# Kernel tuning notes

Measured on AMD Instinct MI355X. Metric: run time of the kernel, lower is better.

The kernel has to match this reference:

```python
import jax, jax.numpy as jnp
import numpy as np

K = 5            # kernel_size
MAX_ORIENT = 8
MAX_LEVEL = 4
D = (K - 1) // 2  # pad amount = 2


def setup_inputs() -> dict:
    key = jax.random.key(0)
    k1, k2, k3 = jax.random.split(key, 3)
    x = jax.random.normal(k1, (32, 1, 512, 512), dtype=jnp.float32)
    fwd_f = jax.random.normal(k2, (MAX_ORIENT, 1, K, K), dtype=jnp.float32)
    fwd_f = fwd_f.at[0, 0].set(jnp.ones((K, K), dtype=jnp.float32))  # per __init__
    inv_f = jax.random.normal(k3, (MAX_ORIENT, 1, K, K), dtype=jnp.float32)
    return {"x": x, "forward_filters": fwd_f, "inverse_filters": inv_f}


def _pad_for_tconv(p):
    # faithful port of padding_for_transpose_conv (static python ints)
    ip, op = 0, 0
    if p > 0:
        op = p
    elif p < 0:
        a = -p
        if a % 2 == 0:
            ip = a // 2
        else:
            op = 1
            ip = (a + 1) // 2
    return ip, op


def _conv2d(x, w, stride, pad):
    # torch F.pad(x, (d,d,d,d)) then conv2d(stride) == conv with symmetric padding
    return jax.lax.conv_general_dilated(
        x, w, window_strides=(stride, stride),
        padding=((pad, pad), (pad, pad)),
        dimension_numbers=("NCHW", "OIHW", "NCHW"))


def _conv_transpose2d(x, w, stride, pad, out_pad):
    # torch conv_transpose2d, weight layout (in_ch, out_ch, kH, kW).
    # Equivalent direct conv: flip kernel spatially, swap I/O axes,
    # lhs_dilation=stride, padding lo=k-1-p, hi=k-1-p+output_padding.
    k = w.shape[2]
    w2 = jnp.transpose(jnp.flip(w, (2, 3)), (1, 0, 2, 3))  # OIHW (1,8,5,5)
    padding = tuple((k - 1 - p, k - 1 - p + op) for p, op in zip(pad, out_pad))
    return jax.lax.conv_general_dilated(
        x, w2, window_strides=(1, 1), padding=padding,
        lhs_dilation=(stride, stride),
        dimension_numbers=("NCHW", "OIHW", "NCHW"))


def _forward_transform(x, fwd_f):
    result = [None] * (MAX_LEVEL + 1)
    vimg = x
    level = MAX_LEVEL
    res = None
    while level > 0 and vimg.shape[2] > 1 and vimg.shape[3] > 1:
        res = _conv2d(vimg, fwd_f, 2, D)   # (B, 8, ceil(H/2)+?, ...)
        result[level] = res
        vimg = res[:, :1]                  # lowpass band feeds next level
        level -= 1
    result[0] = res[:, :1]
    return result


def _inverse_transform(coeffs, inp_dim, inv_f):
    rec = coeffs[0]
    for level in range(1, MAX_LEVEL + 1):
        cur = np.array(coeffs[level].shape[2:])
        target = np.array(inp_dim) if level == MAX_LEVEL else np.array(coeffs[level + 1].shape[2:])
        pc = target - 2 * (cur - 1) - K
        ip0, op0 = _pad_for_tconv(int(pc[0]))
        ip1, op1 = _pad_for_tconv(int(pc[1]))
        full = jnp.concatenate([rec, coeffs[level][:, 1:]], axis=1)  # (B,8,h,w)
        rec = _conv_transpose2d(full, inv_f, 2, (ip0, ip1), (op0, op1))
    return rec


def reference(x, forward_filters, inverse_filters):
    coeffs = _forward_transform(x, forward_filters)
    return _inverse_transform(coeffs, x.shape[2:], inverse_filters)
```

## Files before the change

kernel.cpp:

```cpp
#include <hip/hip_runtime.h>

#define NORIENT 8

__device__ __forceinline__ unsigned xcd_swz(unsigned bid, unsigned nwg) {
    unsigned chunk = nwg >> 3;
    return (nwg & 7u) ? bid : (bid & 7u) * chunk + (bid >> 3);
}

__global__ void fwd_conv_wave_kernel(const float* __restrict__ in, long in_img_stride,
                                     const float* __restrict__ filt,
                                     float* __restrict__ out,
                                     int H, int W, int OH, int OW, int N) {
    constexpr int SROW = 104;
    __shared__ float tile[67 * SROW];

    int nbx = OW >> 5, nby = OH >> 5;
    unsigned sb = xcd_swz(blockIdx.x, gridDim.x);
    int bx = (int)(sb % nbx);
    unsigned t = sb / nbx;
    int by = (int)(t % nby);
    int n = (int)(t / nby);

    const float* __restrict__ ip = in + (long)n * in_img_stride;
    int tid = threadIdx.x;

    int w = __builtin_amdgcn_readfirstlane(tid >> 6);
    const float* __restrict__ F = filt + w * 25;
    float Wt[25];
#pragma unroll
    for (int k = 0; k < 25; ++k) Wt[k] = F[k];

    int gy0 = 64 * by - 2, gx0 = 64 * bx - 4;
#pragma unroll
    for (int k = 0; k < 3; ++k) {
        int e = tid + k * 512;
        if (e < 67 * 18) {
            int row = e / 18, m = e - row * 18;
            int gy = gy0 + row, gx = gx0 + 4 * m;
            bool vl = (gy >= 0) & (gy < H) & (gx >= 0) & (gx <= W - 4);
            float4 val = *(const float4*)(ip + (vl ? ((long)gy * W + gx) : 0));
            float msk = vl ? 1.f : 0.f;
            int off = row * SROW + 4 * m + 4 * (m >> 1);
            *(float4*)&tile[off] = make_float4(val.x * msk, val.y * msk,
                                               val.z * msk, val.w * msk);
        }
    }
    __syncthreads();

    int lane = tid & 63;
    int lx = lane & 7, ly = lane >> 3;

    float acc[4][4];
#pragma unroll
    for (int o = 0; o < 4; ++o)
#pragma unroll
        for (int dx = 0; dx < 4; ++dx) acc[o][dx] = 0.f;

#pragma unroll
    for (int r = 0; r < 11; ++r) {
        int base = (8 * ly + r) * SROW + 12 * lx;
        float4 A = *(const float4*)&tile[base];
        float4 B = *(const float4*)&tile[base + 4];
        float4 C = *(const float4*)&tile[base + 12];
        float4 Dd = *(const float4*)&tile[base + 16];
        float P[16] = {A.x, A.y, A.z, A.w, B.x, B.y, B.z, B.w,
                       C.x, C.y, C.z, C.w, Dd.x, Dd.y, Dd.z, Dd.w};

#pragma unroll
        for (int o = 0; o < 4; ++o) {
            int i = r - 2 * o;
            if (i < 0 || i > 4) continue;
#pragma unroll
            for (int j = 0; j < 5; ++j) {
                float wv = Wt[i * 5 + j];
#pragma unroll
                for (int dx = 0; dx < 4; ++dx)
                    acc[o][dx] = fmaf(P[2 + 2 * dx + j], wv, acc[o][dx]);
            }
        }
    }

    long cs = (long)OH * OW;
    int oy = 32 * by + 4 * ly, ox = 32 * bx + 4 * lx;
    long ob = ((long)n * NORIENT + w) * cs + (long)oy * OW + ox;
#pragma unroll
    for (int o = 0; o < 4; ++o)
        *(float4*)(out + ob + (long)o * OW) =
            make_float4(acc[o][0], acc[o][1], acc[o][2], acc[o][3]);
}

__global__ void inv_tconv_kernel(const float* __restrict__ rec, long rec_img_stride,
                                 const float* __restrict__ coef,
                                 const float* __restrict__ filt,
                                 float* __restrict__ out,
                                 int h, int w, int N) {
    int h2 = h >> 1, w2 = w >> 1;
    unsigned sb = xcd_swz(blockIdx.x, gridDim.x);
    long idx = (long)sb * blockDim.x + threadIdx.x;
    long total = (long)N * h2 * w2;
    if (idx >= total) return;
    int b0 = (int)(idx % w2);
    long t = idx / w2;
    int a0 = (int)(t % h2);
    int n = (int)(t / h2);

    const float* __restrict__ rp = rec + (long)n * rec_img_stride;
    const float* __restrict__ cp = coef + (long)n * (long)NORIENT * h * w;
    long cs = (long)h * w;

    bool fmv = a0 > 0, fpv = a0 < h2 - 1;
    bool um = b0 > 0, up = b0 < w2 - 1;
    float fm = fmv ? 1.f : 0.f, fp_ = fpv ? 1.f : 0.f;
    int r0 = (fmv ? 2 * a0 - 1 : 0) * w;
    int r1 = (2 * a0) * w;
    int r2 = (2 * a0 + 1) * w;
    int r3 = (fpv ? 2 * a0 + 2 : 2 * a0 + 1) * w;
    int cL = um ? 2 * b0 - 2 : 0;
    int cM = 2 * b0;
    int cR = up ? 2 * b0 + 2 : 0;

    float acc[2][2][2][2];
#pragma unroll
    for (int i = 0; i < 2; ++i)
#pragma unroll
        for (int j = 0; j < 2; ++j)
#pragma unroll
            for (int k = 0; k < 2; ++k)
#pragma unroll
                for (int l = 0; l < 2; ++l) acc[i][j][k][l] = 0.f;

    auto do_channel = [&](const float* __restrict__ src, const float* __restrict__ F) {
        float P[4][4];
        const int ro[4] = {r0, r1, r2, r3};
        const float rm[4] = {fm, 1.f, 1.f, fp_};
#pragma unroll
        for (int r = 0; r < 4; ++r) {
            const float* base = src + ro[r];
            float2 L = *(const float2*)(base + cL);
            float2 M = *(const float2*)(base + cM);
            float2 R = *(const float2*)(base + cR);
            float mask = rm[r];
            P[r][0] = (um ? L.y : 0.f) * mask;
            P[r][1] = M.x * mask;
            P[r][2] = M.y * mask;
            P[r][3] = (up ? R.x : 0.f) * mask;
        }
#pragma unroll
        for (int a = 0; a < 3; ++a) {
#pragma unroll
            for (int b = 0; b < 3; ++b) {
                float w00 = F[(4 - 2 * a) * 5 + (4 - 2 * b)];
                float w01 = (b >= 1) ? F[(4 - 2 * a) * 5 + (5 - 2 * b)] : 0.f;
                float w10 = (a >= 1) ? F[(5 - 2 * a) * 5 + (4 - 2 * b)] : 0.f;
                float w11 = (a >= 1 && b >= 1) ? F[(5 - 2 * a) * 5 + (5 - 2 * b)] : 0.f;
#pragma unroll
                for (int sr = 0; sr < 2; ++sr) {
#pragma unroll
                    for (int sc = 0; sc < 2; ++sc) {
                        float pv = P[sr + a][sc + b];
                        acc[sr][sc][0][0] = fmaf(pv, w00, acc[sr][sc][0][0]);
                        if (b >= 1) acc[sr][sc][0][1] = fmaf(pv, w01, acc[sr][sc][0][1]);
                        if (a >= 1) acc[sr][sc][1][0] = fmaf(pv, w10, acc[sr][sc][1][0]);
                        if (a >= 1 && b >= 1)
                                    acc[sr][sc][1][1] = fmaf(pv, w11, acc[sr][sc][1][1]);
                    }
                }
            }
        }
    };

    do_channel(rp, filt);
#pragma unroll
    for (int c = 1; c < NORIENT; ++c)
        do_channel(cp + (long)c * cs, filt + c * 25);

    int OW = w << 1;
    long ob = (long)n * 4 * cs + (long)(4 * a0) * OW + 4 * b0;
    *(float4*)(out + ob)          = make_float4(acc[0][0][0][0], acc[0][0][0][1],
                                                acc[0][1][0][0], acc[0][1][0][1]);
    *(float4*)(out + ob + OW)     = make_float4(acc[0][0][1][0], acc[0][0][1][1],
                                                acc[0][1][1][0], acc[0][1][1][1]);
    *(float4*)(out + ob + 2 * OW) = make_float4(acc[1][0][0][0], acc[1][0][0][1],
                                                acc[1][1][0][0], acc[1][1][0][1]);
    *(float4*)(out + ob + 3 * OW) = make_float4(acc[1][0][1][0], acc[1][0][1][1],
                                                acc[1][1][1][0], acc[1][1][1][1]);
}

extern "C" void kernel_launch(void* const* d_in, const int* in_sizes, int n_in,
                              void* d_out, int out_size, void* d_ws, size_t ws_size,
                              hipStream_t stream) {
    const float* x     = (const float*)d_in[0];
    const float* fwd_f = (const float*)d_in[1];
    const float* inv_f = (const float*)d_in[2];
    float* out = (float*)d_out;
    float* ws  = (float*)d_ws;

    const int N = 32;

    float* l4 = ws;
    float* l3 = l4 + 16777216;
    float* l2 = l3 + 4194304;
    float* l1 = l2 + 1048576;
    float* r1 = l1 + 262144;
    float* r2 = r1 + 131072;
    float* r3 = r2 + 524288;

    dim3 blkF(512), blk(256);
    auto nblocks = [](long total) { return dim3((unsigned)((total + 255) / 256)); };

    fwd_conv_wave_kernel<<<dim3(32 * 8 * 8), blkF, 0, stream>>>(
        x, 512L * 512, fwd_f, l4, 512, 512, 256, 256, N);
    fwd_conv_wave_kernel<<<dim3(32 * 4 * 4), blkF, 0, stream>>>(
        l4, 8L * 256 * 256, fwd_f, l3, 256, 256, 128, 128, N);
    fwd_conv_wave_kernel<<<dim3(32 * 2 * 2), blkF, 0, stream>>>(
        l3, 8L * 128 * 128, fwd_f, l2, 128, 128, 64, 64, N);
    fwd_conv_wave_kernel<<<dim3(32 * 1 * 1), blkF, 0, stream>>>(
        l2, 8L * 64 * 64, fwd_f, l1, 64, 64, 32, 32, N);

    inv_tconv_kernel<<<nblocks(32L * 16 * 16), blk, 0, stream>>>(
        l1, 8L * 32 * 32, l1, inv_f, r1, 32, 32, N);
    inv_tconv_kernel<<<nblocks(32L * 32 * 32), blk, 0, stream>>>(
        r1, 64L * 64, l2, inv_f, r2, 64, 64, N);
    inv_tconv_kernel<<<nblocks(32L * 64 * 64), blk, 0, stream>>>(
        r2, 128L * 128, l3, inv_f, r3, 128, 128, N);
    inv_tconv_kernel<<<nblocks(32L * 128 * 128), blk, 0, stream>>>(
        r3, 256L * 256, l4, inv_f, out, 256, 256, N);
}
```

Before: 96.58 us.

## Fuse last forward level with first inverse level via shared memory

Merges the level-1 forward convolution and the first transposed convolution into one kernel per image, keeping the 8x32x32 coefficients in LDS instead of writing them to global memory. This removes one launch and a global round-trip for a tiny stage that was latency-bound. It also trims the LDS reads in the forward conv to the 11 values actually used. The fused kernel runs only 32 blocks, and its inverse part uses only half the threads.

```diff
diff --git a/kernel.cpp b/kernel.cpp
--- a/kernel.cpp
+++ b/kernel.cpp
@@ -59,12 +59,11 @@
 #pragma unroll
     for (int r = 0; r < 11; ++r) {
         int base = (8 * ly + r) * SROW + 12 * lx;
-        float4 A = *(const float4*)&tile[base];
-        float4 B = *(const float4*)&tile[base + 4];
-        float4 C = *(const float4*)&tile[base + 12];
-        float4 Dd = *(const float4*)&tile[base + 16];
-        float P[16] = {A.x, A.y, A.z, A.w, B.x, B.y, B.z, B.w,
-                       C.x, C.y, C.z, C.w, Dd.x, Dd.y, Dd.z, Dd.w};
+        float2 A2 = *(const float2*)&tile[base + 2];
+        float4 B  = *(const float4*)&tile[base + 4];
+        float4 C  = *(const float4*)&tile[base + 12];
+        float  D  = tile[base + 16];
+        float Q[11] = {A2.x, A2.y, B.x, B.y, B.z, B.w, C.x, C.y, C.z, C.w, D};
 
 #pragma unroll
         for (int o = 0; o < 4; ++o) {
@@ -75,7 +74,7 @@
                 float wv = Wt[i * 5 + j];
 #pragma unroll
                 for (int dx = 0; dx < 4; ++dx)
-                    acc[o][dx] = fmaf(P[2 + 2 * dx + j], wv, acc[o][dx]);
+                    acc[o][dx] = fmaf(Q[2 * dx + j], wv, acc[o][dx]);
             }
         }
     }
@@ -87,6 +86,159 @@
     for (int o = 0; o < 4; ++o)
         *(float4*)(out + ob + (long)o * OW) =
             make_float4(acc[o][0], acc[o][1], acc[o][2], acc[o][3]);
+}
+
+__global__ void fwd4_inv1_fused_kernel(const float* __restrict__ l2,
+                                       const float* __restrict__ fwd_f,
+                                       const float* __restrict__ inv_f,
+                                       float* __restrict__ r1) {
+    constexpr int SROW = 104;
+    __shared__ float tile[67 * SROW];
+    __shared__ float l1t[NORIENT * 32 * 32];
+
+    int n = blockIdx.x;
+    const float* __restrict__ ip = l2 + (long)n * 8 * 64 * 64;
+    int tid = threadIdx.x;
+
+    int w = __builtin_amdgcn_readfirstlane(tid >> 6);
+    {
+        const float* __restrict__ F = fwd_f + w * 25;
+        float Wt[25];
+#pragma unroll
+        for (int k = 0; k < 25; ++k) Wt[k] = F[k];
+
+#pragma unroll
+        for (int k = 0; k < 3; ++k) {
+            int e = tid + k * 512;
+            if (e < 67 * 18) {
+                int row = e / 18, m = e - row * 18;
+                int gy = -2 + row, gx = -4 + 4 * m;
+                bool vl = (gy >= 0) & (gy < 64) & (gx >= 0) & (gx <= 60);
+                float4 val = *(const float4*)(ip + (vl ? ((long)gy * 64 + gx) : 0));
+                float msk = vl ? 1.f : 0.f;
+                int off = row * SROW + 4 * m + 4 * (m >> 1);
+                *(float4*)&tile[off] = make_float4(val.x * msk, val.y * msk,
+                                                   val.z * msk, val.w * msk);
+            }
+        }
+        __syncthreads();
+
+        int lane = tid & 63;
+        int lx = lane & 7, ly = lane >> 3;
+
+        float acc[4][4];
+#pragma unroll
+        for (int o = 0; o < 4; ++o)
+#pragma unroll
+            for (int dx = 0; dx < 4; ++dx) acc[o][dx] = 0.f;
+
+#pragma unroll
+        for (int r = 0; r < 11; ++r) {
+            int base = (8 * ly + r) * SROW + 12 * lx;
+            float2 A2 = *(const float2*)&tile[base + 2];
+            float4 B  = *(const float4*)&tile[base + 4];
+            float4 C  = *(const float4*)&tile[base + 12];
+            float  D  = tile[base + 16];
+            float Q[11] = {A2.x, A2.y, B.x, B.y, B.z, B.w, C.x, C.y, C.z, C.w, D};
+
+#pragma unroll
+            for (int o = 0; o < 4; ++o) {
+                int i = r - 2 * o;
+                if (i < 0 || i > 4) continue;
+#pragma unroll
+                for (int j = 0; j < 5; ++j) {
+                    float wv = Wt[i * 5 + j];
+#pragma unroll
+                    for (int dx = 0; dx < 4; ++dx)
+                        acc[o][dx] = fmaf(Q[2 * dx + j], wv, acc[o][dx]);
+                }
+            }
+        }
+
+#pragma unroll
+        for (int o = 0; o < 4; ++o)
+            *(float4*)&l1t[w * 1024 + (4 * ly + o) * 32 + 4 * lx] =
+                make_float4(acc[o][0], acc[o][1], acc[o][2], acc[o][3]);
+    }
+    __syncthreads();
+
+    if (tid < 256) {
+        int b0 = tid & 15, a0 = tid >> 4;
+
+        bool fmv = a0 > 0, fpv = a0 < 15;
+        bool um = b0 > 0, up = b0 < 15;
+        float fm = fmv ? 1.f : 0.f, fp_ = fpv ? 1.f : 0.f;
+        int r0 = (fmv ? 2 * a0 - 1 : 0) * 32;
+        int r1o = (2 * a0) * 32;
+        int r2o = (2 * a0 + 1) * 32;
+        int r3o = (fpv ? 2 * a0 + 2 : 2 * a0 + 1) * 32;
+        int cL = um ? 2 * b0 - 2 : 0;
+        int cM = 2 * b0;
+        int cR = up ? 2 * b0 + 2 : 0;
+        const int ro[4] = {r0, r1o, r2o, r3o};
+        const float rm[4] = {fm, 1.f, 1.f, fp_};
+
+        float acc[2][2][2][2];
+#pragma unroll
+        for (int i = 0; i < 2; ++i)
+#pragma unroll
+            for (int j = 0; j < 2; ++j)
+#pragma unroll
+                for (int k = 0; k < 2; ++k)
+#pragma unroll
+                    for (int l = 0; l < 2; ++l) acc[i][j][k][l] = 0.f;
+
+#pragma unroll
+        for (int c = 0; c < NORIENT; ++c) {
+            const float* __restrict__ F = inv_f + c * 25;
+            int coff = c * 1024;
+            float P[4][4];
+#pragma unroll
+            for (int r = 0; r < 4; ++r) {
+                int base = coff + ro[r];
+                float2 L = *(const float2*)&l1t[base + cL];
+                float2 M = *(const float2*)&l1t[base + cM];
+                float2 R = *(const float2*)&l1t[base + cR];
+                float mask = rm[r];
+                P[r][0] = (um ? L.y : 0.f) * mask;
+                P[r][1] = M.x * mask;
+                P[r][2] = M.y * mask;
+                P[r][3] = (up ? R.x : 0.f) * mask;
+            }
+#pragma unroll
+            for (int a = 0; a < 3; ++a) {
+#pragma unroll
+                for (int b = 0; b < 3; ++b) {
+                    float w00 = F[(4 - 2 * a) * 5 + (4 - 2 * b)];
+                    float w01 = (b >= 1) ? F[(4 - 2 * a) * 5 + (5 - 2 * b)] : 0.f;
+                    float w10 = (a >= 1) ? F[(5 - 2 * a) * 5 + (4 - 2 * b)] : 0.f;
+                    float w11 = (a >= 1 && b >= 1) ? F[(5 - 2 * a) * 5 + (5 - 2 * b)] : 0.f;
+#pragma unroll
+                    for (int sr = 0; sr < 2; ++sr) {
+#pragma unroll
+                        for (int sc = 0; sc < 2; ++sc) {
+                            float pv = P[sr + a][sc + b];
+                            acc[sr][sc][0][0] = fmaf(pv, w00, acc[sr][sc][0][0]);
+                            if (b >= 1) acc[sr][sc][0][1] = fmaf(pv, w01, acc[sr][sc][0][1]);
+                            if (a >= 1) acc[sr][sc][1][0] = fmaf(pv, w10, acc[sr][sc][1][0]);
+                            if (a >= 1 && b >= 1)
+                                        acc[sr][sc][1][1] = fmaf(pv, w11, acc[sr][sc][1][1]);
+                        }
+                    }
+                }
+            }
+        }
+
+        long ob = (long)n * 4096 + (long)(4 * a0) * 64 + 4 * b0;
+        *(float4*)(r1 + ob)           = make_float4(acc[0][0][0][0], acc[0][0][0][1],
+                                                    acc[0][1][0][0], acc[0][1][0][1]);
+        *(float4*)(r1 + ob + 64)      = make_float4(acc[0][0][1][0], acc[0][0][1][1],
+                                                    acc[0][1][1][0], acc[0][1][1][1]);
+        *(float4*)(r1 + ob + 128)     = make_float4(acc[1][0][0][0], acc[1][0][0][1],
+                                                    acc[1][1][0][0], acc[1][1][0][1]);
+        *(float4*)(r1 + ob + 192)     = make_float4(acc[1][0][1][0], acc[1][0][1][1],
+                                                    acc[1][1][1][0], acc[1][1][1][1]);
+    }
 }
 
 __global__ void inv_tconv_kernel(const float* __restrict__ rec, long rec_img_stride,
@@ -200,8 +352,7 @@
     float* l4 = ws;
     float* l3 = l4 + 16777216;
     float* l2 = l3 + 4194304;
-    float* l1 = l2 + 1048576;
-    float* r1 = l1 + 262144;
+    float* r1 = l2 + 1048576;
     float* r2 = r1 + 131072;
     float* r3 = r2 + 524288;
 
@@ -214,11 +365,9 @@
         l4, 8L * 256 * 256, fwd_f, l3, 256, 256, 128, 128, N);
     fwd_conv_wave_kernel<<<dim3(32 * 2 * 2), blkF, 0, stream>>>(
         l3, 8L * 128 * 128, fwd_f, l2, 128, 128, 64, 64, N);
-    fwd_conv_wave_kernel<<<dim3(32 * 1 * 1), blkF, 0, stream>>>(
-        l2, 8L * 64 * 64, fwd_f, l1, 64, 64, 32, 32, N);
-
-    inv_tconv_kernel<<<nblocks(32L * 16 * 16), blk, 0, stream>>>(
-        l1, 8L * 32 * 32, l1, inv_f, r1, 32, 32, N);
+
+    fwd4_inv1_fused_kernel<<<dim3(32), blkF, 0, stream>>>(l2, fwd_f, inv_f, r1);
+
     inv_tconv_kernel<<<nblocks(32L * 32 * 32), blk, 0, stream>>>(
         r1, 64L * 64, l2, inv_f, r2, 64, 64, N);
     inv_tconv_kernel<<<nblocks(32L * 64 * 64), blk, 0, stream>>>(
```

Measured after the change: 96.77 us. Within noise of the previous version (+0.2%).
